# Performance work log

Hardware: AMD Instinct MI355X
Metric: run time of the kernel (lower is better)

## Reference

```python
import jax, jax.numpy as jnp
import numpy as np

DIM = 256
NUM_HEADS = 8
HEAD_DIM = DIM // NUM_HEADS


def setup_inputs() -> dict:
    key = jax.random.key(0)
    k1, k2, k3, k4 = jax.random.split(key, 4)
    b, n = 4, 2048
    x = jax.random.normal(k1, (b, n, DIM), dtype=jnp.float32)
    # Linear weights with fan-in scaling (matches nn.Linear init magnitude,
    # keeps exp(qk) numerically sane since the original has no max-subtraction).
    Wqkv = jax.random.normal(k2, (DIM, 3 * DIM), dtype=jnp.float32) * (DIM ** -0.5)
    Wout = jax.random.normal(k3, (DIM, DIM), dtype=jnp.float32) * (DIM ** -0.5)
    bout = jax.random.normal(k4, (DIM,), dtype=jnp.float32) * 0.01
    return {"x": x, "Wqkv": Wqkv, "Wout": Wout, "bout": bout}


def reference(x, Wqkv, Wout, bout):
    b, n, d = x.shape
    h, hd = NUM_HEADS, HEAD_DIM
    scale = hd ** -0.5
    qkv = x @ Wqkv  # [b, n, 3d]
    q, k, v = jnp.split(qkv, 3, axis=-1)
    # [b, h, n, hd]
    q = q.reshape(b, n, h, hd).transpose(0, 2, 1, 3) * scale
    k = k.reshape(b, n, h, hd).transpose(0, 2, 1, 3)
    v = v.reshape(b, n, h, hd).transpose(0, 2, 1, 3)
    # Original KeOps path: unnormalized exp (no max-subtraction), separate
    # numerator / denominator reductions, eps in denominator.
    scores = jnp.einsum('bhnd,bhmd->bhnm', q, k)  # [b, h, n, n]
    e = jnp.exp(scores)
    denom = jnp.sum(e, axis=-1, keepdims=True)          # [b, h, n, 1]
    numer = jnp.einsum('bhnm,bhmd->bhnd', e, v)         # [b, h, n, hd]
    out = numer / (denom + 1e-6)
    out = out.transpose(0, 2, 1, 3).reshape(b, n, d)
    return out @ Wout + bout
```

## Files before the change

kernel.cpp:

```cpp
#include <hip/hip_runtime.h>

#define DIM 256
#define NHEADS 8
#define HDIM 32

typedef _Float16 half8_t __attribute__((ext_vector_type(8)));
typedef _Float16 half4_t __attribute__((ext_vector_type(4)));
typedef float float4_t __attribute__((ext_vector_type(4)));

__device__ __forceinline__ void gload_lds16(const void* g, void* l) {
    __builtin_amdgcn_global_load_lds((const __attribute__((address_space(1))) void*)g,
                                     (__attribute__((address_space(3))) void*)l,
                                     16, 0, 0);
}

__global__ __launch_bounds__(256) void prep(const float* __restrict__ x,
                                            const float* __restrict__ Wqkv,
                                            const float* __restrict__ Wout,
                                            _Float16* __restrict__ xh,
                                            _Float16* __restrict__ WqT,
                                            _Float16* __restrict__ WoT) {
    __shared__ float ts[32][33];
    const int bid = blockIdx.x, t = threadIdx.x;
    if (bid < 1024) {
        size_t idx = (size_t)bid * 2048 + (size_t)t * 8;
        float tmp[8];
        *reinterpret_cast<float4*>(tmp)     = *reinterpret_cast<const float4*>(x + idx);
        *reinterpret_cast<float4*>(tmp + 4) = *reinterpret_cast<const float4*>(x + idx + 4);
        half8_t h;
        #pragma unroll
        for (int j = 0; j < 8; ++j) h[j] = (_Float16)tmp[j];
        *reinterpret_cast<half8_t*>(xh + idx) = h;
    } else {
        const float* src; _Float16* dst; int K, N, kb, nb;
        if (bid < 1024 + 192) { int b2 = bid - 1024; src = Wqkv; dst = WqT; K = 256; N = 768; nb = b2 % 24; kb = b2 / 24; }
        else                  { int b3 = bid - 1216; src = Wout; dst = WoT; K = 256; N = 256; nb = b3 % 8;  kb = b3 / 8; }
        const int tx = t & 31, ty = t >> 5;
        #pragma unroll
        for (int i = 0; i < 4; ++i) {
            int k = kb * 32 + ty + i * 8;
            ts[ty + i * 8][tx] = src[(size_t)k * N + nb * 32 + tx];
        }
        __syncthreads();
        #pragma unroll
        for (int i = 0; i < 4; ++i) {
            int nl = ty + i * 8;
            dst[(size_t)(nb * 32 + nl) * K + kb * 32 + tx] = (_Float16)ts[tx][nl];
        }
    }
}

template <bool OUT_HALF, bool VSPLIT>
__global__ __launch_bounds__(256) void gemm_h(const _Float16* __restrict__ A,
                                              const _Float16* __restrict__ BT,
                                              const float* __restrict__ bias,
                                              void* __restrict__ Cv,
                                              _Float16* __restrict__ VTo,
                                              int M, int N, int K, int ldc) {
    __shared__ alignas(16) _Float16 As[128 * 32];
    __shared__ alignas(16) _Float16 Bs[128 * 32];
    const int t = threadIdx.x, lane = t & 63, wave = t >> 6;
    const int l16 = lane & 15, quad = lane >> 4;
    const int m0 = blockIdx.y * 128, n0 = blockIdx.x * 128;
    const int wr = (wave >> 1) * 64, wc = (wave & 1) * 64;
    float4_t acc[4][4];
    #pragma unroll
    for (int i = 0; i < 4; ++i)
        #pragma unroll
        for (int j = 0; j < 4; ++j) acc[i][j] = (float4_t){0.f, 0.f, 0.f, 0.f};

    const int srow = lane >> 2;
    const int scol = (lane & 3) * 8;

    for (int k0 = 0; k0 < K; k0 += 32) {
        #pragma unroll
        for (int i = 0; i < 2; ++i) {
            int chunk = i * 4 + wave;
            int r = chunk * 16 + srow;
            gload_lds16(A  + (size_t)(m0 + r) * K + k0 + scol, As + chunk * 512);
            gload_lds16(BT + (size_t)(n0 + r) * K + k0 + scol, Bs + chunk * 512);
        }
        __syncthreads();
        half8_t af[4], bf[4];
        #pragma unroll
        for (int i = 0; i < 4; ++i)
            af[i] = *reinterpret_cast<const half8_t*>(As + (wr + i * 16 + l16) * 32 + quad * 8);
        #pragma unroll
        for (int j = 0; j < 4; ++j)
            bf[j] = *reinterpret_cast<const half8_t*>(Bs + (wc + j * 16 + l16) * 32 + quad * 8);
        #pragma unroll
        for (int i = 0; i < 4; ++i)
            #pragma unroll
            for (int j = 0; j < 4; ++j)
                acc[i][j] = __builtin_amdgcn_mfma_f32_16x16x32_f16(af[i], bf[j], acc[i][j], 0, 0, 0);
        __syncthreads();
    }

    if (VSPLIT && n0 >= 512) {
        const int bb = m0 >> 11;
        const int tok0 = (m0 & 2047) + wr;
        #pragma unroll
        for (int i = 0; i < 4; ++i)
            #pragma unroll
            for (int j = 0; j < 4; ++j) {
                int vcol = n0 + wc + j * 16 + l16 - 512;
                int hh = vcol >> 5, d = vcol & 31;
                half4_t p;
                #pragma unroll
                for (int r = 0; r < 4; ++r) p[r] = (_Float16)acc[i][j][r];
                *reinterpret_cast<half4_t*>(
                    VTo + ((size_t)(bb * NHEADS + hh) * HDIM + d) * 2048
                        + tok0 + i * 16 + quad * 4) = p;
            }
    } else {
        float bv[4] = {0.f, 0.f, 0.f, 0.f};
        if (bias != nullptr) {
            #pragma unroll
            for (int j = 0; j < 4; ++j) bv[j] = bias[n0 + wc + j * 16 + l16];
        }
        #pragma unroll
        for (int i = 0; i < 4; ++i)
            #pragma unroll
            for (int r = 0; r < 4; ++r) {
                int row = m0 + wr + i * 16 + quad * 4 + r;
                #pragma unroll
                for (int j = 0; j < 4; ++j) {
                    int col = n0 + wc + j * 16 + l16;
                    float v = acc[i][j][r] + bv[j];
                    if (OUT_HALF) ((_Float16*)Cv)[(size_t)row * ldc + col] = (_Float16)v;
                    else          ((float*)Cv)[(size_t)row * ldc + col] = v;
                }
            }
    }
}

__global__ __launch_bounds__(256, 2) void attn_v6(const _Float16* __restrict__ qkh,
                                                  const _Float16* __restrict__ VT,
                                                  _Float16* __restrict__ NUM,
                                                  float* __restrict__ DEN) {
    __shared__ alignas(16) _Float16 es[4][64][40];
    const int bid = blockIdx.x;
    const int kh = bid & 1;
    const int qb = (bid >> 1) & 7;
    const int bh = bid >> 4;
    const int b = bh >> 3, h = bh & 7;
    const int t = threadIdx.x, lane = t & 63, wave = t >> 6;
    const int l16 = lane & 15, quad = lane >> 4;
    const float scale = 0.17677669529663687f;
    const int bN = b * 2048;
    const int q0w = qb * 256 + wave * 64;
    const int kbeg = kh * 1024;

    half8_t qf[4];
    {
        const _Float16* qrow = qkh + (size_t)(bN + q0w + l16) * 512 + h * HDIM + quad * 8;
        #pragma unroll
        for (int g = 0; g < 4; ++g)
            qf[g] = *reinterpret_cast<const half8_t*>(qrow + (size_t)g * 16 * 512);
    }

    const _Float16* kbase = qkh + (size_t)(bN + l16) * 512 + 256 + h * HDIM + quad * 8;
    const _Float16* vbase = VT + (size_t)bh * HDIM * 2048 + (size_t)l16 * 2048 + quad * 8;

    float4_t num[4][2];
    #pragma unroll
    for (int g = 0; g < 4; ++g)
        #pragma unroll
        for (int dt = 0; dt < 2; ++dt) num[g][dt] = (float4_t){0.f, 0.f, 0.f, 0.f};
    float ds[4] = {0.f, 0.f, 0.f, 0.f};
    _Float16* esw = &es[wave][0][0];
    const float4_t z = {0.f, 0.f, 0.f, 0.f};

    for (int k0 = kbeg; k0 < kbeg + 1024; k0 += 64) {
        const _Float16* kp = kbase + (size_t)k0 * 512;
        half8_t kf[4], vf[4];
        #pragma unroll
        for (int j = 0; j < 4; ++j)
            kf[j] = *reinterpret_cast<const half8_t*>(kp + (size_t)j * 16 * 512);
        const _Float16* vp = vbase + k0;
        vf[0] = *reinterpret_cast<const half8_t*>(vp);
        vf[1] = *reinterpret_cast<const half8_t*>(vp + (size_t)16 * 2048);
        vf[2] = *reinterpret_cast<const half8_t*>(vp + 32);
        vf[3] = *reinterpret_cast<const half8_t*>(vp + 32 + (size_t)16 * 2048);

        float4_t st[4][4];
        #pragma unroll
        for (int kb = 0; kb < 4; ++kb)
            #pragma unroll
            for (int g = 0; g < 4; ++g)
                st[kb][g] = __builtin_amdgcn_mfma_f32_16x16x32_f16(kf[kb], qf[g], z, 0, 0, 0);

        half4_t ep[4][4];
        #pragma unroll
        for (int kb = 0; kb < 4; ++kb)
            #pragma unroll
            for (int g = 0; g < 4; ++g)
                #pragma unroll
                for (int r = 0; r < 4; ++r) {
                    float e = __expf(st[kb][g][r] * scale);
                    ds[g] += e;
                    ep[kb][g][r] = (_Float16)e;
                }

        #pragma unroll
        for (int s = 0; s < 2; ++s) {
            #pragma unroll
            for (int tt = 0; tt < 2; ++tt)
                #pragma unroll
                for (int g = 0; g < 4; ++g)
                    *reinterpret_cast<half4_t*>(
                        esw + (g * 16 + l16) * 40 + tt * 16 + quad * 4) = ep[s * 2 + tt][g];

            #pragma unroll
            for (int g = 0; g < 4; ++g) {
                half8_t ef = *reinterpret_cast<const half8_t*>(
                    esw + (g * 16 + l16) * 40 + quad * 8);
                num[g][0] = __builtin_amdgcn_mfma_f32_16x16x32_f16(ef, vf[s * 2],     num[g][0], 0, 0, 0);
                num[g][1] = __builtin_amdgcn_mfma_f32_16x16x32_f16(ef, vf[s * 2 + 1], num[g][1], 0, 0, 0);
            }
        }
    }

    #pragma unroll
    for (int g = 0; g < 4; ++g) {
        ds[g] += __shfl_xor(ds[g], 16, 64);
        ds[g] += __shfl_xor(ds[g], 32, 64);
    }

    _Float16* ob = NUM + (size_t)kh * 2097152 + (size_t)(bN + q0w) * DIM + h * HDIM;
    #pragma unroll
    for (int g = 0; g < 4; ++g)
        #pragma unroll
        for (int r = 0; r < 4; ++r) {
            size_t ro = (size_t)(g * 16 + quad * 4 + r) * DIM;
            ob[ro + l16]      = (_Float16)num[g][0][r];
            ob[ro + 16 + l16] = (_Float16)num[g][1][r];
        }
    if (quad == 0) {
        #pragma unroll
        for (int g = 0; g < 4; ++g)
            DEN[kh * 65536 + bh * 2048 + q0w + g * 16 + l16] = ds[g];
    }
}

__global__ __launch_bounds__(256) void combine(const _Float16* __restrict__ NUM,
                                               const float* __restrict__ DEN,
                                               _Float16* __restrict__ attnh) {
    const size_t idx = ((size_t)blockIdx.x * 256 + threadIdx.x) * 8;
    const int row = (int)(idx >> 8);
    const int c = (int)(idx & 255);
    const int b = row >> 11, tok = row & 2047, h = c >> 5;
    const int di = (b * 8 + h) * 2048 + tok;
    float rcp = 1.0f / (DEN[di] + DEN[di + 65536] + 1e-6f);
    half8_t n0 = *reinterpret_cast<const half8_t*>(NUM + idx);
    half8_t n1 = *reinterpret_cast<const half8_t*>(NUM + idx + 2097152);
    *reinterpret_cast<half8_t*>(attnh + idx) = (n0 + n1) * (_Float16)rcp;
}

extern "C" void kernel_launch(void* const* d_in, const int* in_sizes, int n_in,
                              void* d_out, int out_size, void* d_ws, size_t ws_size,
                              hipStream_t stream) {
    const float* x    = (const float*)d_in[0];
    const float* Wqkv = (const float*)d_in[1];
    const float* Wout = (const float*)d_in[2];
    const float* bout = (const float*)d_in[3];
    float* out = (float*)d_out;
    const int M = 8192;

    _Float16* xh    = (_Float16*)d_ws;
    _Float16* WqT   = xh + (size_t)M * DIM;
    _Float16* WoT   = WqT + 768 * 256;
    _Float16* qkh   = WoT + 256 * 256;
    _Float16* vt    = qkh + (size_t)M * 512;
    _Float16* NUM   = vt + (size_t)32 * HDIM * 2048;
    float*    DEN   = (float*)(NUM + (size_t)2 * M * DIM);
    _Float16* attnh = (_Float16*)(DEN + 2 * 65536);

    hipLaunchKernelGGL(prep, dim3(1280), dim3(256), 0, stream, x, Wqkv, Wout, xh, WqT, WoT);
    hipLaunchKernelGGL((gemm_h<true, true>), dim3(6, 64), dim3(256), 0, stream,
                       xh, WqT, (const float*)nullptr, (void*)qkh, vt, M, 768, DIM, 512);
    hipLaunchKernelGGL(attn_v6, dim3(512), dim3(256), 0, stream, qkh, vt, NUM, DEN);
    hipLaunchKernelGGL(combine, dim3(1024), dim3(256), 0, stream, NUM, DEN, attnh);
    hipLaunchKernelGGL((gemm_h<false, false>), dim3(2, 64), dim3(256), 0, stream,
                       attnh, WoT, bout, (void*)out, (_Float16*)nullptr, M, DIM, DIM, DIM);
}
```

Before: 125.2 us.

## Fold softmax scale into Q projection, use exp2 and MFMA row-sum

The QKV GEMM now multiplies Q by scale*log2(e) in its epilogue, so the attention kernel can call a hardware exp2 directly with no per-element multiply. Exp results are packed to half with cvt_pkrtz. The denominator is now accumulated by an extra MFMA against a vector of ones, using the same fp16 exp values, in place of scalar adds and cross-lane shuffles. The output GEMM is also templated to use 64-row tiles, doubling its grid. This trades VALU work for one extra MFMA per tile, and the sum is now taken over fp16-rounded values.

```diff
diff --git a/kernel.cpp b/kernel.cpp
--- a/kernel.cpp
+++ b/kernel.cpp
@@ -7,6 +7,14 @@
 typedef _Float16 half8_t __attribute__((ext_vector_type(8)));
 typedef _Float16 half4_t __attribute__((ext_vector_type(4)));
 typedef float float4_t __attribute__((ext_vector_type(4)));
+
+__device__ __forceinline__ float fast_exp2(float x) {
+#if __has_builtin(__builtin_amdgcn_exp2f)
+    return __builtin_amdgcn_exp2f(x);
+#else
+    return __expf(x * 0.6931471805599453f);
+#endif
+}
 
 __device__ __forceinline__ void gload_lds16(const void* g, void* l) {
     __builtin_amdgcn_global_load_lds((const __attribute__((address_space(1))) void*)g,
@@ -50,22 +58,24 @@
     }
 }
 
-template <bool OUT_HALF, bool VSPLIT>
+template <bool OUT_HALF, bool VSPLIT, int MROWS>
 __global__ __launch_bounds__(256) void gemm_h(const _Float16* __restrict__ A,
                                               const _Float16* __restrict__ BT,
                                               const float* __restrict__ bias,
                                               void* __restrict__ Cv,
                                               _Float16* __restrict__ VTo,
                                               int M, int N, int K, int ldc) {
-    __shared__ alignas(16) _Float16 As[128 * 32];
+    constexpr int BM = MROWS * 32;
+    __shared__ alignas(16) _Float16 As[BM * 32];
     __shared__ alignas(16) _Float16 Bs[128 * 32];
     const int t = threadIdx.x, lane = t & 63, wave = t >> 6;
     const int l16 = lane & 15, quad = lane >> 4;
-    const int m0 = blockIdx.y * 128, n0 = blockIdx.x * 128;
-    const int wr = (wave >> 1) * 64, wc = (wave & 1) * 64;
-    float4_t acc[4][4];
-    #pragma unroll
-    for (int i = 0; i < 4; ++i)
+    const int m0 = blockIdx.y * BM, n0 = blockIdx.x * 128;
+    const int wr = (wave >> 1) * (MROWS * 16), wc = (wave & 1) * 64;
+    constexpr float QS = 0.17677669529663687f * 1.4426950408889634f;
+    float4_t acc[MROWS][4];
+    #pragma unroll
+    for (int i = 0; i < MROWS; ++i)
         #pragma unroll
         for (int j = 0; j < 4; ++j) acc[i][j] = (float4_t){0.f, 0.f, 0.f, 0.f};
 
@@ -73,23 +83,28 @@
     const int scol = (lane & 3) * 8;
 
     for (int k0 = 0; k0 < K; k0 += 32) {
+        #pragma unroll
+        for (int i = 0; i < MROWS / 2; ++i) {
+            int chunk = i * 4 + wave;
+            int r = chunk * 16 + srow;
+            gload_lds16(A + (size_t)(m0 + r) * K + k0 + scol, As + chunk * 512);
+        }
         #pragma unroll
         for (int i = 0; i < 2; ++i) {
             int chunk = i * 4 + wave;
             int r = chunk * 16 + srow;
-            gload_lds16(A  + (size_t)(m0 + r) * K + k0 + scol, As + chunk * 512);
             gload_lds16(BT + (size_t)(n0 + r) * K + k0 + scol, Bs + chunk * 512);
         }
         __syncthreads();
-        half8_t af[4], bf[4];
-        #pragma unroll
-        for (int i = 0; i < 4; ++i)
+        half8_t af[MROWS], bf[4];
+        #pragma unroll
+        for (int i = 0; i < MROWS; ++i)
             af[i] = *reinterpret_cast<const half8_t*>(As + (wr + i * 16 + l16) * 32 + quad * 8);
         #pragma unroll
         for (int j = 0; j < 4; ++j)
             bf[j] = *reinterpret_cast<const half8_t*>(Bs + (wc + j * 16 + l16) * 32 + quad * 8);
         #pragma unroll
-        for (int i = 0; i < 4; ++i)
+        for (int i = 0; i < MROWS; ++i)
             #pragma unroll
             for (int j = 0; j < 4; ++j)
                 acc[i][j] = __builtin_amdgcn_mfma_f32_16x16x32_f16(af[i], bf[j], acc[i][j], 0, 0, 0);
@@ -100,7 +115,7 @@
         const int bb = m0 >> 11;
         const int tok0 = (m0 & 2047) + wr;
         #pragma unroll
-        for (int i = 0; i < 4; ++i)
+        for (int i = 0; i < MROWS; ++i)
             #pragma unroll
             for (int j = 0; j < 4; ++j) {
                 int vcol = n0 + wc + j * 16 + l16 - 512;
@@ -119,7 +134,7 @@
             for (int j = 0; j < 4; ++j) bv[j] = bias[n0 + wc + j * 16 + l16];
         }
         #pragma unroll
-        for (int i = 0; i < 4; ++i)
+        for (int i = 0; i < MROWS; ++i)
             #pragma unroll
             for (int r = 0; r < 4; ++r) {
                 int row = m0 + wr + i * 16 + quad * 4 + r;
@@ -127,6 +142,7 @@
                 for (int j = 0; j < 4; ++j) {
                     int col = n0 + wc + j * 16 + l16;
                     float v = acc[i][j][r] + bv[j];
+                    if (VSPLIT && n0 < 256) v *= QS;
                     if (OUT_HALF) ((_Float16*)Cv)[(size_t)row * ldc + col] = (_Float16)v;
                     else          ((float*)Cv)[(size_t)row * ldc + col] = v;
                 }
@@ -134,7 +150,7 @@
     }
 }
 
-__global__ __launch_bounds__(256, 2) void attn_v6(const _Float16* __restrict__ qkh,
+__global__ __launch_bounds__(256, 2) void attn_v7(const _Float16* __restrict__ qkh,
                                                   const _Float16* __restrict__ VT,
                                                   _Float16* __restrict__ NUM,
                                                   float* __restrict__ DEN) {
@@ -146,7 +162,6 @@
     const int b = bh >> 3, h = bh & 7;
     const int t = threadIdx.x, lane = t & 63, wave = t >> 6;
     const int l16 = lane & 15, quad = lane >> 4;
-    const float scale = 0.17677669529663687f;
     const int bN = b * 2048;
     const int q0w = qb * 256 + wave * 64;
     const int kbeg = kh * 1024;
@@ -167,7 +182,14 @@
     for (int g = 0; g < 4; ++g)
         #pragma unroll
         for (int dt = 0; dt < 2; ++dt) num[g][dt] = (float4_t){0.f, 0.f, 0.f, 0.f};
-    float ds[4] = {0.f, 0.f, 0.f, 0.f};
+    float4_t dacc[4];
+    #pragma unroll
+    for (int g = 0; g < 4; ++g) dacc[g] = (float4_t){0.f, 0.f, 0.f, 0.f};
+
+    half8_t onef;
+    #pragma unroll
+    for (int j = 0; j < 8; ++j) onef[j] = (_Float16)1.0f;
+
     _Float16* esw = &es[wave][0][0];
     const float4_t z = {0.f, 0.f, 0.f, 0.f};
 
@@ -183,24 +205,17 @@
         vf[2] = *reinterpret_cast<const half8_t*>(vp + 32);
         vf[3] = *reinterpret_cast<const half8_t*>(vp + 32 + (size_t)16 * 2048);
 
-        float4_t st[4][4];
+        half4_t ep[4][4];
         #pragma unroll
         for (int kb = 0; kb < 4; ++kb)
             #pragma unroll
-            for (int g = 0; g < 4; ++g)
-                st[kb][g] = __builtin_amdgcn_mfma_f32_16x16x32_f16(kf[kb], qf[g], z, 0, 0, 0);
-
-        half4_t ep[4][4];
-        #pragma unroll
-        for (int kb = 0; kb < 4; ++kb)
-            #pragma unroll
-            for (int g = 0; g < 4; ++g)
-                #pragma unroll
-                for (int r = 0; r < 4; ++r) {
-                    float e = __expf(st[kb][g][r] * scale);
-                    ds[g] += e;
-                    ep[kb][g][r] = (_Float16)e;
-                }
+            for (int g = 0; g < 4; ++g) {
+                float4_t st = __builtin_amdgcn_mfma_f32_16x16x32_f16(kf[kb], qf[g], z, 0, 0, 0);
+                auto lo = __builtin_amdgcn_cvt_pkrtz(fast_exp2(st[0]), fast_exp2(st[1]));
+                auto hi = __builtin_amdgcn_cvt_pkrtz(fast_exp2(st[2]), fast_exp2(st[3]));
+                ep[kb][g] = (half4_t){(_Float16)lo[0], (_Float16)lo[1],
+                                      (_Float16)hi[0], (_Float16)hi[1]};
+            }
 
         #pragma unroll
         for (int s = 0; s < 2; ++s) {
@@ -217,14 +232,9 @@
                     esw + (g * 16 + l16) * 40 + quad * 8);
                 num[g][0] = __builtin_amdgcn_mfma_f32_16x16x32_f16(ef, vf[s * 2],     num[g][0], 0, 0, 0);
                 num[g][1] = __builtin_amdgcn_mfma_f32_16x16x32_f16(ef, vf[s * 2 + 1], num[g][1], 0, 0, 0);
-            }
-        }
-    }
-
-    #pragma unroll
-    for (int g = 0; g < 4; ++g) {
-        ds[g] += __shfl_xor(ds[g], 16, 64);
-        ds[g] += __shfl_xor(ds[g], 32, 64);
+                dacc[g]   = __builtin_amdgcn_mfma_f32_16x16x32_f16(ef, onef,          dacc[g],   0, 0, 0);
+            }
+        }
     }
 
     _Float16* ob = NUM + (size_t)kh * 2097152 + (size_t)(bN + q0w) * DIM + h * HDIM;
@@ -236,10 +246,12 @@
             ob[ro + l16]      = (_Float16)num[g][0][r];
             ob[ro + 16 + l16] = (_Float16)num[g][1][r];
         }
-    if (quad == 0) {
+    if (l16 == 0) {
         #pragma unroll
         for (int g = 0; g < 4; ++g)
-            DEN[kh * 65536 + bh * 2048 + q0w + g * 16 + l16] = ds[g];
+            #pragma unroll
+            for (int r = 0; r < 4; ++r)
+                DEN[kh * 65536 + bh * 2048 + q0w + g * 16 + quad * 4 + r] = dacc[g][r];
     }
 }
 
@@ -277,10 +289,10 @@
     _Float16* attnh = (_Float16*)(DEN + 2 * 65536);
 
     hipLaunchKernelGGL(prep, dim3(1280), dim3(256), 0, stream, x, Wqkv, Wout, xh, WqT, WoT);
-    hipLaunchKernelGGL((gemm_h<true, true>), dim3(6, 64), dim3(256), 0, stream,
+    hipLaunchKernelGGL((gemm_h<true, true, 4>), dim3(6, 64), dim3(256), 0, stream,
                        xh, WqT, (const float*)nullptr, (void*)qkh, vt, M, 768, DIM, 512);
-    hipLaunchKernelGGL(attn_v6, dim3(512), dim3(256), 0, stream, qkh, vt, NUM, DEN);
+    hipLaunchKernelGGL(attn_v7, dim3(512), dim3(256), 0, stream, qkh, vt, NUM, DEN);
     hipLaunchKernelGGL(combine, dim3(1024), dim3(256), 0, stream, NUM, DEN, attnh);
-    hipLaunchKernelGGL((gemm_h<false, false>), dim3(2, 64), dim3(256), 0, stream,
+    hipLaunchKernelGGL((gemm_h<false, false, 2>), dim3(2, 128), dim3(256), 0, stream,
                        attnh, WoT, bout, (void*)out, (_Float16*)nullptr, M, DIM, DIM, DIM);
 }
```

Result: no change. 127.2 us (+1.6%).
